# Optimization experiments

Hardware: AMD Instinct MI355X
Metric: run time of the kernel (lower is better)

The kernel has to match this reference:

```python
import jax, jax.numpy as jnp
import numpy as np

B, S, H = 8, 2048, 512

def setup_inputs() -> dict:
    key = jax.random.key(0)
    k1, k2, k3 = jax.random.split(key, 3)
    O = jax.random.normal(k1, (B, S, H), dtype=jnp.float32)
    # torch Linear default init ~ U(-1/sqrt(H), 1/sqrt(H)); scale randn similarly
    Wa_w = jax.random.normal(k2, (H, H), dtype=jnp.float32) / jnp.sqrt(jnp.float32(H))
    Wa_b = jax.random.normal(k3, (H,), dtype=jnp.float32) / jnp.sqrt(jnp.float32(H))
    return {"O": O, "Wa_w": Wa_w, "Wa_b": Wa_b}

def reference(O, Wa_w, Wa_b):
    # Q = tanh(O @ Wa_w^T + b)   (torch Linear convention: y = x W^T + b)
    Q = jnp.tanh(jnp.einsum('bsh,oh->bso', O, Wa_w) + Wa_b)
    # scores = Q @ O^T  -> (B, S, S)
    scores = jnp.einsum('bsh,bth->bst', Q, O)
    a = jax.nn.softmax(scores, axis=-1)
    # Oa = a @ O -> (B, S, H)
    Oa = jnp.einsum('bst,bth->bsh', a, O)
    return Oa
```

## Files before the change

### kernel.cpp

```cpp
#include <hip/hip_runtime.h>
#include <cmath>

typedef _Float16 f16;
typedef _Float16 f16x8 __attribute__((ext_vector_type(8)));
typedef float    f32x4 __attribute__((ext_vector_type(4)));
typedef unsigned short u16;
typedef unsigned int   u32;
typedef u16 us8 __attribute__((ext_vector_type(8)));
typedef u16 us4 __attribute__((ext_vector_type(4)));

#define MFMA16(a, b, c) __builtin_amdgcn_mfma_f32_16x16x32_f16((a), (b), (c), 0, 0, 0)

__device__ __forceinline__ void gload_lds16(const void* g, void* l) {
    __builtin_amdgcn_global_load_lds((const __attribute__((address_space(1))) void*)g,
                                     (__attribute__((address_space(3))) void*)l, 16, 0, 0);
}

__global__ void castk(const float* __restrict__ src, f16* __restrict__ dst, int n8) {
    int i = blockIdx.x * 256 + threadIdx.x;
    if (i >= n8) return;
    const float4* s = (const float4*)src + (size_t)i * 2;
    float4 a = s[0], b = s[1];
    union { f16 h[8]; us8 v; } o;
    o.h[0] = (f16)a.x; o.h[1] = (f16)a.y; o.h[2] = (f16)a.z; o.h[3] = (f16)a.w;
    o.h[4] = (f16)b.x; o.h[5] = (f16)b.y; o.h[6] = (f16)b.z; o.h[7] = (f16)b.w;
    *(us8*)&dst[(size_t)i * 8] = o.v;
}

__global__ void prep(const float* __restrict__ O, f16* __restrict__ Of16,
                     f16* __restrict__ OT) {
    __shared__ f16 tbuf[64][68];
    int bid = blockIdx.x;
    int b = bid >> 8, t = bid & 255;
    int s0 = (t & 31) * 64, h0 = (t >> 5) * 64;
    const float* Ob = O + (size_t)b * 2048 * 512;
    f16* Ofb = Of16 + (size_t)b * 2048 * 512;
    f16* OTb = OT + (size_t)b * 512 * 2048;
    int tid = threadIdx.x;
    int rr = tid >> 4, cc = (tid & 15) * 4;
#pragma unroll
    for (int i = 0; i < 4; ++i) {
        int r = rr + 16 * i;
        float4 v = *(const float4*)&Ob[(size_t)(s0 + r) * 512 + h0 + cc];
        union { f16 h[4]; us4 u; } st;
        st.h[0] = (f16)v.x; st.h[1] = (f16)v.y; st.h[2] = (f16)v.z; st.h[3] = (f16)v.w;
        *(us4*)&Ofb[(size_t)(s0 + r) * 512 + h0 + cc] = st.u;
        tbuf[r][cc + 0] = st.h[0]; tbuf[r][cc + 1] = st.h[1];
        tbuf[r][cc + 2] = st.h[2]; tbuf[r][cc + 3] = st.h[3];
    }
    __syncthreads();
#pragma unroll
    for (int i = 0; i < 4; ++i) {
        int hr = rr + 16 * i;
        union { f16 h[4]; us4 v; } pk;
        pk.h[0] = tbuf[cc + 0][hr]; pk.h[1] = tbuf[cc + 1][hr];
        pk.h[2] = tbuf[cc + 2][hr]; pk.h[3] = tbuf[cc + 3][hr];
        *(us4*)&OTb[(size_t)(h0 + hr) * 2048 + s0 + cc] = pk.v;
    }
}

__global__ __launch_bounds__(256) void gemm1(const f16* __restrict__ A,
                                             const f16* __restrict__ W,
                                             const float* __restrict__ bias,
                                             f16* __restrict__ Qo) {
    __shared__ f16 lA[128 * 32];
    __shared__ f16 lB[128 * 32];
    const int tid = threadIdx.x;
    const int lane = tid & 63, w = tid >> 6;
    const int wm = w >> 1, wn = w & 1;
    const int bm = blockIdx.x >> 2, bn = blockIdx.x & 3;
    const int r0 = bm * 128, c0 = bn * 128;
    const int l15 = lane & 15, g = lane >> 4;
    f32x4 acc[4][4] = {};
    for (int kt = 0; kt < 16; ++kt) {
        int k0 = kt * 32;
        __syncthreads();
#pragma unroll
        for (int i = 0; i < 2; ++i) {
            int slot = i * 256 + tid;
            int row = slot >> 2, oct = slot & 3;
            int soct = oct ^ (row & 3);
            *(us8*)&lA[slot * 8] = *(const us8*)&A[(size_t)(r0 + row) * 512 + k0 + soct * 8];
            *(us8*)&lB[slot * 8] = *(const us8*)&W[(size_t)(c0 + row) * 512 + k0 + soct * 8];
        }
        __syncthreads();
        f16x8 af[4], bf[4];
#pragma unroll
        for (int mf = 0; mf < 4; ++mf) {
            int row = 64 * wm + 16 * mf + l15;
            int oct = g ^ (row & 3);
            af[mf] = *(const f16x8*)&lA[(row * 4 + oct) * 8];
        }
#pragma unroll
        for (int nf = 0; nf < 4; ++nf) {
            int row = 64 * wn + 16 * nf + l15;
            int oct = g ^ (row & 3);
            bf[nf] = *(const f16x8*)&lB[(row * 4 + oct) * 8];
        }
#pragma unroll
        for (int mf = 0; mf < 4; ++mf)
#pragma unroll
            for (int nf = 0; nf < 4; ++nf)
                acc[mf][nf] = MFMA16(af[mf], bf[nf], acc[mf][nf]);
    }
    float bv[4];
#pragma unroll
    for (int nf = 0; nf < 4; ++nf) bv[nf] = bias[c0 + 64 * wn + 16 * nf + l15];
#pragma unroll
    for (int mf = 0; mf < 4; ++mf) {
#pragma unroll
        for (int nf = 0; nf < 4; ++nf) {
#pragma unroll
            for (int r = 0; r < 4; ++r) {
                float y = tanhf(acc[mf][nf][r] + bv[nf]);
                int row = r0 + 64 * wm + 16 * mf + 4 * g + r;
                int col = c0 + 64 * wn + 16 * nf + l15;
                Qo[(size_t)row * 512 + col] = (f16)y;
            }
        }
    }
}

__global__ __launch_bounds__(512, 2) void attn(const f16* __restrict__ Qf,
                                               const f16* __restrict__ Of,
                                               const f16* __restrict__ OfT,
                                               float* __restrict__ P0,
                                               f16* __restrict__ P1,
                                               float* __restrict__ ML) {
    extern __shared__ __align__(16) char smem[];
    const int tid = threadIdx.x;
    const int lane = tid & 63, w = tid >> 6;
    const int l15 = lane & 15, g = lane >> 4;
    const int b = blockIdx.x & 7, tt = (blockIdx.x >> 3) & 1, qt = blockIdx.x >> 4;
    const int q0 = qt * 128;
    const int tb = tt * 1024;
    const f16* Ob  = Of  + (size_t)b * 2048 * 512;
    const f16* OTb = OfT + (size_t)b * 512 * 2048;

    f16x8 qf[16];
    const f16* qrow = Qf + ((size_t)b * 2048 + q0 + 16 * w + l15) * 512;
#pragma unroll
    for (int ks = 0; ks < 16; ++ks) qf[ks] = *(const f16x8*)&qrow[ks * 32 + g * 8];

    float m = -INFINITY, lsum = 0.f;
    f32x4 acc[32] = {};

    const int addrA = 4 * (32 * (g & 1) + l15);
    const int addrB = addrA + 64;
    const int kx = (l15 & 3) ^ ((l15 >> 2) & 3);
    const int go = g ^ kx;

    auto STAGE_K = [&](int buf, int t0) {
        f16* dst = (f16*)(smem + buf * 32768);
#pragma unroll
        for (int i = 0; i < 4; ++i) {
            int slot = i * 512 + tid;
            int t = slot >> 6, oct = slot & 63;
            gload_lds16(&Ob[(size_t)(t0 + t) * 512 + 8 * (oct ^ (t & 7))], &dst[slot * 8]);
        }
    };
    auto STAGE_V = [&](int buf, int t0) {
        f16* dst = (f16*)(smem + 65536 + buf * 32768);
#pragma unroll
        for (int i = 0; i < 4; ++i) {
            int slot = i * 512 + tid;
            int h = slot >> 2, gr = slot & 3;
            int key = (h & 3) ^ ((h >> 2) & 3);
            gload_lds16(&OTb[(size_t)h * 2048 + t0 + 8 * (gr ^ key)], &dst[slot * 8]);
        }
    };

    STAGE_K(0, tb);
    STAGE_V(0, tb);

    for (int kt = 0; kt < 32; ++kt) {
        const int cur = kt & 1;
        const f16* lK = (const f16*)(smem + cur * 32768);
        const f16* lV = (const f16*)(smem + 65536 + cur * 32768);

        if (kt < 31) {
            STAGE_K(cur ^ 1, tb + (kt + 1) * 32);
            STAGE_V(cur ^ 1, tb + (kt + 1) * 32);
            asm volatile("s_waitcnt vmcnt(8)" ::: "memory");
        } else {
            asm volatile("s_waitcnt vmcnt(0)" ::: "memory");
        }
        __builtin_amdgcn_s_barrier();

        f32x4 sa[2] = {};
#pragma unroll
        for (int ks = 0; ks < 16; ++ks) {
#pragma unroll
            for (int mf = 0; mf < 2; ++mf) {
                int t = 16 * mf + l15;
                int oct = (4 * ks + g) ^ (t & 7);
                f16x8 kf = *(const f16x8*)&lK[(t * 64 + oct) * 8];
                sa[mf] = MFMA16(kf, qf[ks], sa[mf]);
            }
        }

        float tmax = -INFINITY;
#pragma unroll
        for (int mf = 0; mf < 2; ++mf)
#pragma unroll
            for (int r = 0; r < 4; ++r) tmax = fmaxf(tmax, sa[mf][r]);
        tmax = fmaxf(tmax, __shfl_xor(tmax, 16));
        tmax = fmaxf(tmax, __shfl_xor(tmax, 32));
        if (__any(tmax > m + 8.0f)) {
            float mnew = fmaxf(m, tmax);
            float corr = __expf(m - mnew);
            m = mnew;
            lsum *= corr;
#pragma unroll
            for (int hf = 0; hf < 32; ++hf) acc[hf] *= corr;
        }
        float p[2][4];
        float ps = 0.f;
#pragma unroll
        for (int mf = 0; mf < 2; ++mf)
#pragma unroll
            for (int r = 0; r < 4; ++r) { p[mf][r] = __expf(sa[mf][r] - m); ps += p[mf][r]; }
        ps += __shfl_xor(ps, 16);
        ps += __shfl_xor(ps, 32);
        lsum += ps;

        u32 Wd[2][2];
#pragma unroll
        for (int mf = 0; mf < 2; ++mf)
#pragma unroll
            for (int c = 0; c < 2; ++c) {
                union { f16 h[2]; u32 u; } x;
                x.h[0] = (f16)p[mf][2 * c]; x.h[1] = (f16)p[mf][2 * c + 1];
                Wd[mf][c] = x.u;
            }
        u32 word[4];
#pragma unroll
        for (int pp = 0; pp < 4; ++pp) {
            int adr = (pp >> 1) ? addrB : addrA;
            int w0 = __builtin_amdgcn_ds_bpermute(adr, (int)Wd[0][pp & 1]);
            int w1 = __builtin_amdgcn_ds_bpermute(adr, (int)Wd[1][pp & 1]);
            word[pp] = (lane >= 32) ? (u32)w1 : (u32)w0;
        }
        union { u32 u[4]; f16x8 v; } pkk;
        pkk.u[0] = word[0]; pkk.u[1] = word[1]; pkk.u[2] = word[2]; pkk.u[3] = word[3];
        f16x8 pfrag = pkk.v;

#pragma unroll
        for (int hf = 0; hf < 32; ++hf) {
            int h = 16 * hf + l15;
            f16x8 vf = *(const f16x8*)&lV[(h * 4 + go) * 8];
            acc[hf] = MFMA16(vf, pfrag, acc[hf]);
        }

        asm volatile("s_waitcnt lgkmcnt(0)" ::: "memory");
        __builtin_amdgcn_s_barrier();
    }

    const size_t row = (size_t)b * 2048 + q0 + 16 * w + l15;
    if (g == 0) {
        ML[(tt * 16384 + row) * 2 + 0] = m;
        ML[(tt * 16384 + row) * 2 + 1] = lsum;
    }
    if (tt == 0) {
#pragma unroll
        for (int hf = 0; hf < 32; ++hf) {
            float4 o;
            o.x = acc[hf][0]; o.y = acc[hf][1];
            o.z = acc[hf][2]; o.w = acc[hf][3];
            *(float4*)&P0[row * 512 + 16 * hf + 4 * g] = o;
        }
    } else {
        float inv = 1.0f / lsum;
#pragma unroll
        for (int hf = 0; hf < 32; ++hf) {
            union { f16 h[4]; us4 v; } pk;
            pk.h[0] = (f16)(acc[hf][0] * inv); pk.h[1] = (f16)(acc[hf][1] * inv);
            pk.h[2] = (f16)(acc[hf][2] * inv); pk.h[3] = (f16)(acc[hf][3] * inv);
            *(us4*)&P1[row * 512 + 16 * hf + 4 * g] = pk.v;
        }
    }
}

__global__ __launch_bounds__(256) void merge_k(float* __restrict__ P0,
                                               const f16* __restrict__ P1,
                                               const float* __restrict__ ML) {
    const int tid = threadIdx.x;
    const size_t row = (size_t)blockIdx.x * 8 + (tid >> 5);
    const int c = (tid & 31) * 16;
    float m0 = ML[row * 2 + 0], l0 = ML[row * 2 + 1];
    float m1 = ML[(16384 + row) * 2 + 0], l1 = ML[(16384 + row) * 2 + 1];
    float M = fmaxf(m0, m1);
    float e0 = __expf(m0 - M), e1 = __expf(m1 - M);
    float w1 = e1 * l1;
    float inv = 1.0f / (e0 * l0 + w1);
    float a0 = e0 * inv, a1 = w1 * inv;
#pragma unroll
    for (int j = 0; j < 4; ++j) {
        size_t off = row * 512 + c + 4 * j;
        float4 v0 = *(const float4*)&P0[off];
        us4 v1u = *(const us4*)&P1[off];
        const f16* v1 = (const f16*)&v1u;
        float4 o;
        o.x = a0 * v0.x + a1 * (float)v1[0];
        o.y = a0 * v0.y + a1 * (float)v1[1];
        o.z = a0 * v0.z + a1 * (float)v1[2];
        o.w = a0 * v0.w + a1 * (float)v1[3];
        *(float4*)&P0[off] = o;
    }
}

extern "C" void kernel_launch(void* const* d_in, const int* in_sizes, int n_in,
                              void* d_out, int out_size, void* d_ws, size_t ws_size,
                              hipStream_t stream) {
    const float* O  = (const float*)d_in[0];
    const float* Ww = (const float*)d_in[1];
    const float* Wb = (const float*)d_in[2];
    float* Out = (float*)d_out;
    char* ws = (char*)d_ws;
    f16* Of16 = (f16*)ws;
    f16* OT   = (f16*)(ws + ((size_t)16 << 20));
    f16* Qf   = (f16*)(ws + ((size_t)32 << 20));
    f16* Wf   = (f16*)(ws + ((size_t)48 << 20));
    f16* P1   = (f16*)(ws + ((size_t)49 << 20));
    float* ML = (float*)(ws + ((size_t)65 << 20));

    hipFuncSetAttribute((const void*)attn, hipFuncAttributeMaxDynamicSharedMemorySize, 131072);

    prep<<<2048, 256, 0, stream>>>(O, Of16, OT);
    castk<<<128, 256, 0, stream>>>(Ww, Wf, 32768);
    gemm1<<<512, 256, 0, stream>>>(Of16, Wf, Wb, Qf);
    attn<<<256, 512, 131072, stream>>>(Qf, Of16, OT, Out, P1, ML);
    merge_k<<<2048, 256, 0, stream>>>(Out, P1, ML);
}
```

Baseline: 170.0 us.

## Double-buffer gemm1 LDS tiles with async global-to-LDS loads

The Q-projection GEMM now uses two LDS buffers and issues direct global-to-LDS loads for the next K tile before computing on the current one. It waits with vmcnt and s_barrier instead of a synchronous load-then-sync pattern. The aim is to overlap global memory latency with MFMA work. It doubles shared memory use, which may reduce occupancy, and it relies on hand-placed waitcnt counts that must stay correct.

Measured after the change: 167.9 us. Within noise of the previous version (-1.2%).

```diff
diff --git a/kernel.cpp b/kernel.cpp
--- a/kernel.cpp
+++ b/kernel.cpp
@@ -63,8 +63,8 @@
                                              const f16* __restrict__ W,
                                              const float* __restrict__ bias,
                                              f16* __restrict__ Qo) {
-    __shared__ f16 lA[128 * 32];
-    __shared__ f16 lB[128 * 32];
+    __shared__ f16 lA[2 * 128 * 32];
+    __shared__ f16 lB[2 * 128 * 32];
     const int tid = threadIdx.x;
     const int lane = tid & 63, w = tid >> 6;
     const int wm = w >> 1, wn = w & 1;
@@ -72,36 +72,54 @@
     const int r0 = bm * 128, c0 = bn * 128;
     const int l15 = lane & 15, g = lane >> 4;
     f32x4 acc[4][4] = {};
-    for (int kt = 0; kt < 16; ++kt) {
-        int k0 = kt * 32;
-        __syncthreads();
+
+    auto STAGE = [&](int buf, int k0) {
+        f16* dA = lA + buf * 4096;
+        f16* dB = lB + buf * 4096;
 #pragma unroll
         for (int i = 0; i < 2; ++i) {
             int slot = i * 256 + tid;
             int row = slot >> 2, oct = slot & 3;
             int soct = oct ^ (row & 3);
-            *(us8*)&lA[slot * 8] = *(const us8*)&A[(size_t)(r0 + row) * 512 + k0 + soct * 8];
-            *(us8*)&lB[slot * 8] = *(const us8*)&W[(size_t)(c0 + row) * 512 + k0 + soct * 8];
-        }
-        __syncthreads();
+            gload_lds16(&A[(size_t)(r0 + row) * 512 + k0 + soct * 8], &dA[slot * 8]);
+            gload_lds16(&W[(size_t)(c0 + row) * 512 + k0 + soct * 8], &dB[slot * 8]);
+        }
+    };
+
+    STAGE(0, 0);
+    for (int kt = 0; kt < 16; ++kt) {
+        const int cur = kt & 1;
+        if (kt < 15) {
+            STAGE(cur ^ 1, (kt + 1) * 32);
+            asm volatile("s_waitcnt vmcnt(4)" ::: "memory");
+        } else {
+            asm volatile("s_waitcnt vmcnt(0)" ::: "memory");
+        }
+        __builtin_amdgcn_s_barrier();
+
+        const f16* cA = lA + cur * 4096;
+        const f16* cB = lB + cur * 4096;
         f16x8 af[4], bf[4];
 #pragma unroll
         for (int mf = 0; mf < 4; ++mf) {
             int row = 64 * wm + 16 * mf + l15;
             int oct = g ^ (row & 3);
-            af[mf] = *(const f16x8*)&lA[(row * 4 + oct) * 8];
+            af[mf] = *(const f16x8*)&cA[(row * 4 + oct) * 8];
         }
 #pragma unroll
         for (int nf = 0; nf < 4; ++nf) {
             int row = 64 * wn + 16 * nf + l15;
             int oct = g ^ (row & 3);
-            bf[nf] = *(const f16x8*)&lB[(row * 4 + oct) * 8];
+            bf[nf] = *(const f16x8*)&cB[(row * 4 + oct) * 8];
         }
 #pragma unroll
         for (int mf = 0; mf < 4; ++mf)
 #pragma unroll
             for (int nf = 0; nf < 4; ++nf)
                 acc[mf][nf] = MFMA16(af[mf], bf[nf], acc[mf][nf]);
+
+        asm volatile("s_waitcnt lgkmcnt(0)" ::: "memory");
+        __builtin_amdgcn_s_barrier();
     }
     float bv[4];
 #pragma unroll
```
